# Performance work log

Measured on AMD Instinct MI355X. Metric: run time of the kernel, lower is better.

## Reference

```python
import jax, jax.numpy as jnp
import numpy as np

ROPE_THETA = 10000.0

def _rope(x, offset=0):
    # x: [B, H, T, d]; lucidrains rotary_embedding_torch interleaved-pair convention
    d = x.shape[-1]
    T = x.shape[-2]
    inv_freq = 1.0 / (ROPE_THETA ** (jnp.arange(0, d, 2, dtype=jnp.float32) / d))  # [d/2]
    t = jnp.arange(offset, offset + T, dtype=jnp.float32)
    freqs = t[:, None] * inv_freq[None, :]                 # [T, d/2]
    freqs = jnp.repeat(freqs, 2, axis=-1)                  # [T, d] (each freq duplicated for its pair)
    cos = jnp.cos(freqs).astype(x.dtype)
    sin = jnp.sin(freqs).astype(x.dtype)
    xr = x.reshape(*x.shape[:-1], d // 2, 2)
    x1, x2 = xr[..., 0], xr[..., 1]
    rot = jnp.stack([-x2, x1], axis=-1).reshape(x.shape)   # rotate_half, interleaved
    return x * cos + rot * sin


def setup_inputs() -> dict:
    key = jax.random.key(0)
    ks = jax.random.split(key, 5)
    B, T, C = 8, 1024, 1024
    s = 0.02
    x = jax.random.normal(ks[0], (B, T, C), dtype=jnp.float32)
    ipw = jax.random.normal(ks[1], (3 * C, C), dtype=jnp.float32) * s
    ipb = jax.random.normal(ks[2], (3 * C,), dtype=jnp.float32) * s
    opw = jax.random.normal(ks[3], (C, C), dtype=jnp.float32) * s
    opb = jax.random.normal(ks[4], (C,), dtype=jnp.float32) * s
    # bool mask, True = blocked (original code inverts before SDPA) -> causal
    causal_block = ~jnp.tril(jnp.ones((T, T), dtype=bool))
    attn_mask = causal_block[None, None, :, :]             # [1,1,T,T]
    return {"x": x, "ipw": ipw, "ipb": ipb, "opw": opw, "opb": opb,
            "attn_mask": attn_mask}


def reference(x, ipw, ipb, opw, opb, attn_mask):
    B, T, C = x.shape
    n_head = 16
    hd = C // n_head
    qkv = x @ ipw.T + ipb                                  # [B,T,3C]
    q, k, v = jnp.split(qkv, 3, axis=-1)
    def heads(z):
        return z.reshape(B, T, n_head, hd).transpose(0, 2, 1, 3)  # [B,H,T,hd]
    q, k, v = heads(q), heads(k), heads(v)
    q = _rope(q)
    k = _rope(k)
    scores = jnp.einsum('bhqd,bhkd->bhqk', q, k) / jnp.sqrt(jnp.asarray(hd, x.dtype))
    # attn_mask True = blocked; mask slice [FULL_T-T:FULL_T, :FULL_T] is the full mask here
    scores = jnp.where(attn_mask, jnp.asarray(-1e9, x.dtype), scores)
    attn = jax.nn.softmax(scores, axis=-1)
    y = jnp.einsum('bhqk,bhkd->bhqd', attn, v)             # [B,H,T,hd]
    y = y.transpose(0, 2, 1, 3).reshape(B, T, C)
    return y @ opw.T + opb
```

## Files before the change

kernel.cpp:

```cpp
#include <hip/hip_runtime.h>
#include <stdint.h>


typedef __bf16 bf16x8 __attribute__((ext_vector_type(8)));
typedef float f32x4 __attribute__((ext_vector_type(4)));
typedef __attribute__((address_space(1))) unsigned int as1_u32;
typedef __attribute__((address_space(3))) unsigned int as3_u32;

#define MFMA16(a, b, c) __builtin_amdgcn_mfma_f32_16x16x32_bf16((a), (b), (c), 0, 0, 0)

static __device__ __forceinline__ unsigned short f2bf(float f) {
    union { float f; unsigned u; } x; x.f = f;
    return (unsigned short)((x.u + 0x7fffu + ((x.u >> 16) & 1u)) >> 16);
}
static __device__ __forceinline__ float bf2f(unsigned short u) {
    union { unsigned u; float f; } x; x.u = ((unsigned)u) << 16;
    return x.f;
}
static __device__ __forceinline__ bf16x8 ld_bf16x8(const void* p) {
    return *(const bf16x8*)p;
}
static __device__ __forceinline__ unsigned cvtpk(float lo, float hi) {
    unsigned r;
    asm("v_cvt_pk_bf16_f32 %0, %1, %2" : "=v"(r) : "v"(lo), "v"(hi));
    return r;
}

__global__ void cast_f32_bf16(const float* __restrict__ in,
                              unsigned short* __restrict__ out, int n8) {
    int i = blockIdx.x * blockDim.x + threadIdx.x;
    if (i >= n8) return;
    float4 a = ((const float4*)in)[2 * i];
    float4 b = ((const float4*)in)[2 * i + 1];
    union { unsigned short us[8]; uint4 v; } o;
    o.us[0] = f2bf(a.x); o.us[1] = f2bf(a.y); o.us[2] = f2bf(a.z); o.us[3] = f2bf(a.w);
    o.us[4] = f2bf(b.x); o.us[5] = f2bf(b.y); o.us[6] = f2bf(b.z); o.us[7] = f2bf(b.w);
    ((uint4*)out)[i] = o.v;
}

__global__ void rope_table(float* __restrict__ ct, float* __restrict__ st) {
    int idx = blockIdx.x * blockDim.x + threadIdx.x;
    if (idx >= 1024 * 32) return;
    int t = idx >> 5, i = idx & 31;
    float inv = powf(10000.0f, -(float)(2 * i) * (1.0f / 64.0f));
    float f = (float)t * inv;
    ct[idx] = cosf(f);
    st[idx] = sinf(f);
}

__global__ __launch_bounds__(512, 2) void gemm1_8ph(const unsigned short* __restrict__ A,
                                                    const unsigned short* __restrict__ W,
                                                    const float* __restrict__ bias,
                                                    unsigned short* __restrict__ Cout) {
    __shared__ __attribute__((aligned(16))) char lds[131072];
    constexpr int NH = 32;
    constexpr int NTN = 12;

    int nwg = gridDim.x;
    int bid = blockIdx.x;
    int lg = (bid & 7) * (nwg >> 3) + (bid >> 3);
    int tm = lg / NTN, tn = lg % NTN;
    int m0 = tm * 256, n0 = tn * 256;

    int tid = threadIdx.x;
    int w = tid >> 6, l = tid & 63;
    int lr = l & 15, g = l >> 4;
    int wm = w >> 2, wn = w & 3;
    int ldsb = __builtin_amdgcn_readfirstlane(w * 1024);

    auto srcoff = [](int c) {
        int row = c >> 3;
        int sl = (c & 7) ^ (row & 7);
        int rg = (row << 1) | (sl >> 2);
        int cg = (sl & 3) * 8;
        return rg * 1024 + cg;
    };
    int c0 = tid, c1 = tid + 512;
    const unsigned short* pA0 = A + (size_t)m0 * 1024 + srcoff(c0);
    const unsigned short* pA1 = A + (size_t)m0 * 1024 + srcoff(c1);
    const unsigned short* pB0 = W + (size_t)n0 * 1024 + srcoff(c0);
    const unsigned short* pB1 = W + (size_t)n0 * 1024 + srcoff(c1);

    int lr2 = lr >> 1;
    int sst16 = ((((lr & 1) << 2) + g) ^ lr2) << 4;
    int aBase = (wm * 64 + lr2) * 128 + sst16;
    int bBase = (wn * 32 + lr2) * 128 + sst16;

    f32x4 acc[8][4] = {};

    for (int js = 0; js < 3; ++js) {
        char* Ad = lds + js * 16384;
        char* Bd = lds + 65536 + js * 16384;
        __builtin_amdgcn_global_load_lds((const as1_u32*)(pA0 + js * 32), (as3_u32*)(Ad + ldsb), 16, 0, 0);
        __builtin_amdgcn_global_load_lds((const as1_u32*)(pA1 + js * 32), (as3_u32*)(Ad + 8192 + ldsb), 16, 0, 0);
        __builtin_amdgcn_global_load_lds((const as1_u32*)(pB0 + js * 32), (as3_u32*)(Bd + ldsb), 16, 0, 0);
        __builtin_amdgcn_global_load_lds((const as1_u32*)(pB1 + js * 32), (as3_u32*)(Bd + 8192 + ldsb), 16, 0, 0);
    }
    asm volatile("s_waitcnt vmcnt(8)" ::: "memory");
    __builtin_amdgcn_s_barrier();

#pragma unroll 4
    for (int j = 0; j < NH; ++j) {
        const char* Asl = lds + (j & 3) * 16384;
        const char* Bsl = lds + 65536 + (j & 3) * 16384;
        int js = j + 3;
        char* Ad = lds + (js & 3) * 16384;
        char* Bd = lds + 65536 + (js & 3) * 16384;
        bf16x8 aa[4], bb[4];

#pragma unroll
        for (int fn = 0; fn < 4; ++fn) bb[fn] = ld_bf16x8(Bsl + bBase + fn * 1024);
#pragma unroll
        for (int fm = 0; fm < 4; ++fm) aa[fm] = ld_bf16x8(Asl + aBase + fm * 1024);
        if (js < NH) {
            __builtin_amdgcn_global_load_lds((const as1_u32*)(pA0 + js * 32), (as3_u32*)(Ad + ldsb), 16, 0, 0);
            __builtin_amdgcn_global_load_lds((const as1_u32*)(pA1 + js * 32), (as3_u32*)(Ad + 8192 + ldsb), 16, 0, 0);
        }
        __builtin_amdgcn_s_barrier();
        __builtin_amdgcn_s_setprio(1);
#pragma unroll
        for (int fm = 0; fm < 4; ++fm)
#pragma unroll
            for (int fn = 0; fn < 4; ++fn) acc[fm][fn] = MFMA16(aa[fm], bb[fn], acc[fm][fn]);
        __builtin_amdgcn_s_setprio(0);
        __builtin_amdgcn_s_barrier();

#pragma unroll
        for (int fm = 0; fm < 4; ++fm) aa[fm] = ld_bf16x8(Asl + aBase + (fm + 4) * 1024);
        if (js < NH) {
            __builtin_amdgcn_global_load_lds((const as1_u32*)(pB0 + js * 32), (as3_u32*)(Bd + ldsb), 16, 0, 0);
            __builtin_amdgcn_global_load_lds((const as1_u32*)(pB1 + js * 32), (as3_u32*)(Bd + 8192 + ldsb), 16, 0, 0);
        }
        __builtin_amdgcn_s_barrier();
        __builtin_amdgcn_s_setprio(1);
#pragma unroll
        for (int fm = 0; fm < 4; ++fm)
#pragma unroll
            for (int fn = 0; fn < 4; ++fn) acc[fm + 4][fn] = MFMA16(aa[fm], bb[fn], acc[fm + 4][fn]);
        __builtin_amdgcn_s_setprio(0);
        if (j + 3 < NH)      asm volatile("s_waitcnt vmcnt(8)" ::: "memory");
        else if (j + 2 < NH) asm volatile("s_waitcnt vmcnt(4)" ::: "memory");
        else if (j + 1 < NH) asm volatile("s_waitcnt vmcnt(0)" ::: "memory");
        __builtin_amdgcn_s_barrier();
    }

#pragma unroll
    for (int fn = 0; fn < 4; ++fn) {
        int col = n0 + wn * 64 + fn * 16 + lr;
        float bv = bias[col];
#pragma unroll
        for (int fm = 0; fm < 8; ++fm) {
            int row = m0 + wm * 128 + fm * 16 + g * 4;
#pragma unroll
            for (int r = 0; r < 4; ++r)
                Cout[(size_t)(row + r) * 3072 + col] = f2bf(acc[fm][fn][r] + bv);
        }
    }
}

template <int NC, bool OUT_BF16>
__global__ __launch_bounds__(256) void gemm_bt(const unsigned short* __restrict__ A,
                                               const unsigned short* __restrict__ W,
                                               const float* __restrict__ bias,
                                               void* __restrict__ Cout, int K) {
    __shared__ __attribute__((aligned(16))) unsigned short As[128 * 32];
    __shared__ __attribute__((aligned(16))) unsigned short Bs[128 * 32];

    constexpr int NT = NC / 128;
    int nwg = gridDim.x;
    int bid = blockIdx.x;
    int lg = (bid & 7) * (nwg >> 3) + (bid >> 3);
    int tm = lg / NT, tn = lg % NT;
    int m0 = tm * 128, n0 = tn * 128;

    int tid = threadIdx.x;
    int w = tid >> 6, l = tid & 63;
    int lr = l & 15, g = l >> 4;
    int ldsb = __builtin_amdgcn_readfirstlane(w * 512);

    int c0 = tid, c1 = tid + 256;
    const unsigned short* A0 = A + (size_t)(m0 + (c0 >> 2)) * K + (c0 & 3) * 8;
    const unsigned short* A1 = A + (size_t)(m0 + (c1 >> 2)) * K + (c1 & 3) * 8;
    const unsigned short* W0 = W + (size_t)(n0 + (c0 >> 2)) * K + (c0 & 3) * 8;
    const unsigned short* W1 = W + (size_t)(n0 + (c1 >> 2)) * K + (c1 & 3) * 8;

    f32x4 acc[4][4] = {};
    int wr = (w >> 1) * 64, wc = (w & 1) * 64;

    for (int k0 = 0; k0 < K; k0 += 32) {
        __syncthreads();
        __builtin_amdgcn_global_load_lds((const as1_u32*)(A0 + k0), (as3_u32*)(As + ldsb), 16, 0, 0);
        __builtin_amdgcn_global_load_lds((const as1_u32*)(A1 + k0), (as3_u32*)(As + 2048 + ldsb), 16, 0, 0);
        __builtin_amdgcn_global_load_lds((const as1_u32*)(W0 + k0), (as3_u32*)(Bs + ldsb), 16, 0, 0);
        __builtin_amdgcn_global_load_lds((const as1_u32*)(W1 + k0), (as3_u32*)(Bs + 2048 + ldsb), 16, 0, 0);
        __syncthreads();

        bf16x8 a[4], b[4];
#pragma unroll
        for (int i = 0; i < 4; ++i) a[i] = ld_bf16x8(As + (wr + i * 16 + lr) * 32 + g * 8);
#pragma unroll
        for (int j = 0; j < 4; ++j) b[j] = ld_bf16x8(Bs + (wc + j * 16 + lr) * 32 + g * 8);
#pragma unroll
        for (int i = 0; i < 4; ++i)
#pragma unroll
            for (int j = 0; j < 4; ++j) acc[i][j] = MFMA16(a[i], b[j], acc[i][j]);
    }

    int g4 = g * 4;
#pragma unroll
    for (int j = 0; j < 4; ++j) {
        int col = n0 + wc + j * 16 + lr;
        float bv = bias[col];
#pragma unroll
        for (int i = 0; i < 4; ++i) {
#pragma unroll
            for (int r = 0; r < 4; ++r) {
                int row = m0 + wr + i * 16 + g4 + r;
                float v = acc[i][j][r] + bv;
                if (OUT_BF16)
                    ((unsigned short*)Cout)[(size_t)row * NC + col] = f2bf(v);
                else
                    ((float*)Cout)[(size_t)row * NC + col] = v;
            }
        }
    }
}

__global__ void rope_reshape(const unsigned short* __restrict__ qkv,
                             const float* __restrict__ ct, const float* __restrict__ st,
                             unsigned short* __restrict__ Qh,
                             unsigned short* __restrict__ Kh) {
    int idx = blockIdx.x * blockDim.x + threadIdx.x;
    if (idx >= 8192 * 256) return;
    int row = idx >> 8;
    int col = (idx & 255) * 8;
    int sec = col >> 10;
    int wi = col & 1023;
    int h = wi >> 6, d = wi & 63;
    int t = row & 1023;

    uint4 raw = *(const uint4*)(qkv + (size_t)row * 3072 + col);
    size_t obase = ((size_t)((row >> 10) * 16 + h) * 1024 + t) * 64 + d;

    union { uint4 v; unsigned short us[8]; } u; u.v = raw;
    float x[8];
#pragma unroll
    for (int i = 0; i < 8; ++i) x[i] = bf2f(u.us[i]);
    float scale = (sec == 0) ? 0.125f : 1.0f;
    union { uint4 v; unsigned short us[8]; } o;
#pragma unroll
    for (int p = 0; p < 4; ++p) {
        int fi = t * 32 + (d >> 1) + p;
        float c = ct[fi], s = st[fi];
        float e0 = (x[2 * p] * c - x[2 * p + 1] * s) * scale;
        float e1 = (x[2 * p + 1] * c + x[2 * p] * s) * scale;
        o.us[2 * p] = f2bf(e0);
        o.us[2 * p + 1] = f2bf(e1);
    }
    unsigned short* dst = (sec == 0) ? Qh : Kh;
    *(uint4*)(dst + obase) = o.v;
}

__global__ __launch_bounds__(256) void transpose_v(const unsigned short* __restrict__ qkv,
                                                   unsigned short* __restrict__ Vt) {
    __shared__ unsigned short Ts[64 * 67];
    int bid = blockIdx.x;
    int bh = bid >> 4, tt = bid & 15;
    int b = bh >> 4, h = bh & 15;
    int t0 = tt * 64;
    int tid = threadIdx.x;
#pragma unroll
    for (int cc = 0; cc < 2; ++cc) {
        int c = tid + cc * 256;
        int trow = c >> 3, d8 = (c & 7) * 8;
        uint4 v = *(const uint4*)(qkv + (size_t)(b * 1024 + t0 + trow) * 3072 + 2048 + h * 64 + d8);
        union { uint4 v; unsigned short us[8]; } u; u.v = v;
#pragma unroll
        for (int i = 0; i < 8; ++i) Ts[trow * 67 + d8 + i] = u.us[i];
    }
    __syncthreads();
#pragma unroll
    for (int cc = 0; cc < 2; ++cc) {
        int c = tid + cc * 256;
        int drow = c >> 3, t8 = (c & 7) * 8;
        union { uint4 v; unsigned short us[8]; } u;
#pragma unroll
        for (int i = 0; i < 8; ++i) u.us[i] = Ts[(t8 + i) * 67 + drow];
        *(uint4*)(Vt + (size_t)bh * 65536 + (size_t)drow * 1024 + t0 + t8) = u.v;
    }
}

__device__ __forceinline__ void attn_tile(const unsigned short* Ks, const unsigned short* Vs,
                                          bf16x8 q0f, bf16x8 q1f, f32x4 (&y)[4],
                                          float& rm, float& rl,
                                          int lr, int g, bool diag, int wq) {
    const char* kc = (const char*)Ks;
    const char* vc = (const char*)Vs;
    int l7 = lr & 7;
    int kof0 = lr * 128 + ((g ^ l7) << 4);
    int kof1 = lr * 128 + (((g + 4) ^ l7) << 4);
    f32x4 s[4];
#pragma unroll
    for (int nt = 0; nt < 4; ++nt) {
        bf16x8 kf0 = ld_bf16x8(kc + nt * 2048 + kof0);
        bf16x8 kf1 = ld_bf16x8(kc + nt * 2048 + kof1);
        f32x4 z = {};
        z = MFMA16(kf0, q0f, z);
        z = MFMA16(kf1, q1f, z);
        s[nt] = z;
    }
    if (diag) {
#pragma unroll
        for (int nt = 0; nt < 4; ++nt)
#pragma unroll
            for (int r = 0; r < 4; ++r)
                if (nt * 16 + g * 4 + r > wq + lr) s[nt][r] = -3e38f;
    }
    float tm;
    {
        f32x4 m4;
#pragma unroll
        for (int r = 0; r < 4; ++r) m4[r] = fmaxf(fmaxf(s[0][r], s[1][r]), fmaxf(s[2][r], s[3][r]));
        tm = fmaxf(fmaxf(m4[0], m4[1]), fmaxf(m4[2], m4[3]));
    }
    tm = fmaxf(tm, __shfl_xor(tm, 16));
    tm = fmaxf(tm, __shfl_xor(tm, 32));
    float nm = fmaxf(rm, tm);
    float alpha = __expf(rm - nm);
    rm = nm;
    float ts = 0.f;
#pragma unroll
    for (int nt = 0; nt < 4; ++nt)
#pragma unroll
        for (int r = 0; r < 4; ++r) { float pv = __expf(s[nt][r] - nm); s[nt][r] = pv; ts += pv; }
    ts += __shfl_xor(ts, 16);
    ts += __shfl_xor(ts, 32);
    rl = rl * alpha + ts;
#pragma unroll
    for (int nt = 0; nt < 4; ++nt) y[nt] *= alpha;
    union { unsigned u[4]; bf16x8 v; } pf0, pf1;
    pf0.u[0] = cvtpk(s[0][0], s[0][1]); pf0.u[1] = cvtpk(s[0][2], s[0][3]);
    pf0.u[2] = cvtpk(s[1][0], s[1][1]); pf0.u[3] = cvtpk(s[1][2], s[1][3]);
    pf1.u[0] = cvtpk(s[2][0], s[2][1]); pf1.u[1] = cvtpk(s[2][2], s[2][3]);
    pf1.u[2] = cvtpk(s[3][0], s[3][1]); pf1.u[3] = cvtpk(s[3][2], s[3][3]);
    int s0 = g >> 1, h8 = (g & 1) * 8;
    int vo0 = lr * 128 + h8 + (((s0 + 0) ^ l7) << 4);
    int vo1 = lr * 128 + h8 + (((s0 + 2) ^ l7) << 4);
    int vo2 = lr * 128 + h8 + (((s0 + 4) ^ l7) << 4);
    int vo3 = lr * 128 + h8 + (((s0 + 6) ^ l7) << 4);
#pragma unroll
    for (int nt = 0; nt < 4; ++nt) {
        union { uint2 u2[2]; bf16x8 v; } vf;
        vf.u2[0] = *(const uint2*)(vc + nt * 2048 + vo0);
        vf.u2[1] = *(const uint2*)(vc + nt * 2048 + vo1);
        y[nt] = MFMA16(vf.v, pf0.v, y[nt]);
        union { uint2 u2[2]; bf16x8 v; } vg;
        vg.u2[0] = *(const uint2*)(vc + nt * 2048 + vo2);
        vg.u2[1] = *(const uint2*)(vc + nt * 2048 + vo3);
        y[nt] = MFMA16(vg.v, pf1.v, y[nt]);
    }
}

__device__ __forceinline__ void attn_epilogue(unsigned short* smem, unsigned short* __restrict__ Yb,
                                              f32x4 (&y)[4], float rl, int qtile,
                                              int b, int hh, int w, int lr, int g, int tid) {
    __syncthreads();
    float inv = 1.0f / rl;
    char* ep = (char*)smem;
#pragma unroll
    for (int nt = 0; nt < 4; ++nt) {
        uint2 pr;
        pr.x = cvtpk(y[nt][0] * inv, y[nt][1] * inv);
        pr.y = cvtpk(y[nt][2] * inv, y[nt][3] * inv);
        *(uint2*)(ep + (w * 16 + lr) * 144 + (nt * 16 + g * 4) * 2) = pr;
    }
    __syncthreads();
    int q = tid >> 2, dc = (tid & 3) * 16;
    uint4 u0 = *(const uint4*)(ep + q * 144 + dc * 2);
    uint4 u1 = *(const uint4*)(ep + q * 144 + dc * 2 + 16);
    size_t orow = ((size_t)(b * 1024 + qtile * 64 + q)) * 1024 + hh * 64 + dc;
    *(uint4*)(Yb + orow) = u0;
    *(uint4*)(Yb + orow + 8) = u1;
}

__global__ __launch_bounds__(256) void attn_fwd(const unsigned short* __restrict__ Qh,
                                                const unsigned short* __restrict__ Kh,
                                                const unsigned short* __restrict__ Vt,
                                                unsigned short* __restrict__ Yb) {
    __shared__ __attribute__((aligned(16))) unsigned short smem[8192];
    unsigned short* Ks = smem;
    unsigned short* Vs = smem + 4096;

    int bid = blockIdx.x;
    int lg = (bid & 7) * 128 + (bid >> 3);
    int bh = lg >> 3, p = lg & 7;
    int qa = p, qb = 15 - p;

    int tid = threadIdx.x, w = tid >> 6, l = tid & 63;
    int lr = l & 15, g = l >> 4;
    int ldsb = __builtin_amdgcn_readfirstlane(w * 512);

    size_t bh64 = (size_t)bh * 65536;
    const unsigned short* qbase = Qh + bh64 + (size_t)(w * 16 + lr) * 64 + g * 8;
    bf16x8 qA0 = ld_bf16x8(qbase + qa * 4096);
    bf16x8 qA1 = ld_bf16x8(qbase + qa * 4096 + 32);
    bf16x8 qB0 = ld_bf16x8(qbase + qb * 4096);
    bf16x8 qB1 = ld_bf16x8(qbase + qb * 4096 + 32);

    f32x4 yA[4] = {}, yB[4] = {};
    float mA = -3e38f, lA = 0.f, mB = -3e38f, lB = 0.f;

    int c0 = tid, c1 = tid + 256;
    const unsigned short* K0 = Kh + bh64 + (c0 >> 3) * 64 + ((c0 ^ (c0 >> 3)) & 7) * 8;
    const unsigned short* K1 = Kh + bh64 + (c1 >> 3) * 64 + ((c1 ^ (c1 >> 3)) & 7) * 8;
    const unsigned short* V0 = Vt + bh64 + (c0 >> 3) * 1024 + ((c0 ^ (c0 >> 3)) & 7) * 8;
    const unsigned short* V1 = Vt + bh64 + (c1 >> 3) * 1024 + ((c1 ^ (c1 >> 3)) & 7) * 8;

    for (int t = 0; t <= qb; ++t) {
        __syncthreads();
        __builtin_amdgcn_global_load_lds((const as1_u32*)(K0 + t * 4096), (as3_u32*)(Ks + ldsb), 16, 0, 0);
        __builtin_amdgcn_global_load_lds((const as1_u32*)(K1 + t * 4096), (as3_u32*)(Ks + 2048 + ldsb), 16, 0, 0);
        __builtin_amdgcn_global_load_lds((const as1_u32*)(V0 + t * 64), (as3_u32*)(Vs + ldsb), 16, 0, 0);
        __builtin_amdgcn_global_load_lds((const as1_u32*)(V1 + t * 64), (as3_u32*)(Vs + 2048 + ldsb), 16, 0, 0);
        __syncthreads();

        if (t <= qa)
            attn_tile(Ks, Vs, qA0, qA1, yA, mA, lA, lr, g, t == qa, w * 16);
        attn_tile(Ks, Vs, qB0, qB1, yB, mB, lB, lr, g, t == qb, w * 16);
    }

    int b = bh >> 4, hh = bh & 15;
    attn_epilogue(smem, Yb, yA, lA, qa, b, hh, w, lr, g, tid);
    attn_epilogue(smem, Yb, yB, lB, qb, b, hh, w, lr, g, tid);
}

extern "C" void kernel_launch(void* const* d_in, const int* in_sizes, int n_in,
                              void* d_out, int out_size, void* d_ws, size_t ws_size,
                              hipStream_t stream) {
    const float* x = (const float*)d_in[0];
    const float* ipw = (const float*)d_in[1];
    const float* ipb = (const float*)d_in[2];
    const float* opw = (const float*)d_in[3];
    const float* opb = (const float*)d_in[4];

    char* ws = (char*)d_ws;
    unsigned short* xb   = (unsigned short*)(ws);
    unsigned short* wqkv = (unsigned short*)(ws + 16777216);
    unsigned short* wo   = (unsigned short*)(ws + 23068672);
    float* ct            = (float*)(ws + 25165824);
    float* st            = (float*)(ws + 25296896);
    unsigned short* qkvb = (unsigned short*)(ws + 25427968);
    unsigned short* Qh   = (unsigned short*)(ws + 75759616);
    unsigned short* Kh   = (unsigned short*)(ws + 92536832);
    unsigned short* Vt   = (unsigned short*)(ws + 109314048);
    unsigned short* yb   = (unsigned short*)(ws + 126091264);

    cast_f32_bf16<<<4096, 256, 0, stream>>>(x, xb, 1048576);
    cast_f32_bf16<<<1536, 256, 0, stream>>>(ipw, wqkv, 393216);
    cast_f32_bf16<<<512, 256, 0, stream>>>(opw, wo, 131072);
    rope_table<<<128, 256, 0, stream>>>(ct, st);

    gemm1_8ph<<<384, 512, 0, stream>>>(xb, wqkv, ipb, qkvb);
    rope_reshape<<<8192, 256, 0, stream>>>(qkvb, ct, st, Qh, Kh);
    transpose_v<<<2048, 256, 0, stream>>>(qkvb, Vt);
    attn_fwd<<<1024, 256, 0, stream>>>(Qh, Kh, Vt, yb);
    gemm_bt<1024, false><<<512, 256, 0, stream>>>(yb, wo, opb, d_out, 1024);
}
```

Before: 277.3 us.

## Widen QKV GEMM tile to 256x384 with triple-buffered LDS and staged epilogue

The QKV projection GEMM tile grows from 256x256 to 256x384, cutting the grid from 384 to 256 workgroups, which matches the 256 CUs, and raising MFMA work per A-fragment load. LDS buffering changes from a 4-slot ring to 3 rotating buffers to fit the larger B tile. The epilogue now stages bf16 results through swizzled LDS so it can issue 16-byte coalesced global stores instead of scattered 2-byte stores. The cost is more accumulator registers (48 f32x4 per thread), which adds register pressure and can hurt occupancy, plus only two k-steps of prefetch in flight.

```diff
diff --git a/kernel.cpp b/kernel.cpp
--- a/kernel.cpp
+++ b/kernel.cpp
@@ -52,15 +52,14 @@
                                                     const unsigned short* __restrict__ W,
                                                     const float* __restrict__ bias,
                                                     unsigned short* __restrict__ Cout) {
-    __shared__ __attribute__((aligned(16))) char lds[131072];
+    __shared__ __attribute__((aligned(16))) char lds[122880];
     constexpr int NH = 32;
-    constexpr int NTN = 12;
 
     int nwg = gridDim.x;
     int bid = blockIdx.x;
     int lg = (bid & 7) * (nwg >> 3) + (bid >> 3);
-    int tm = lg / NTN, tn = lg % NTN;
-    int m0 = tm * 256, n0 = tn * 256;
+    int tm = lg >> 3, tn = lg & 7;
+    int m0 = tm * 256, n0 = tn * 384;
 
     int tid = threadIdx.x;
     int w = tid >> 6, l = tid & 63;
@@ -75,85 +74,104 @@
         int cg = (sl & 3) * 8;
         return rg * 1024 + cg;
     };
-    int c0 = tid, c1 = tid + 512;
-    const unsigned short* pA0 = A + (size_t)m0 * 1024 + srcoff(c0);
-    const unsigned short* pA1 = A + (size_t)m0 * 1024 + srcoff(c1);
-    const unsigned short* pB0 = W + (size_t)n0 * 1024 + srcoff(c0);
-    const unsigned short* pB1 = W + (size_t)n0 * 1024 + srcoff(c1);
+    const unsigned short* pA0 = A + (size_t)m0 * 1024 + srcoff(tid);
+    const unsigned short* pA1 = A + (size_t)m0 * 1024 + srcoff(tid + 512);
+    const unsigned short* pB0 = W + (size_t)n0 * 1024 + srcoff(tid);
+    const unsigned short* pB1 = W + (size_t)n0 * 1024 + srcoff(tid + 512);
+    const unsigned short* pB2 = W + (size_t)n0 * 1024 + srcoff(tid + 1024);
 
     int lr2 = lr >> 1;
     int sst16 = ((((lr & 1) << 2) + g) ^ lr2) << 4;
     int aBase = (wm * 64 + lr2) * 128 + sst16;
-    int bBase = (wn * 32 + lr2) * 128 + sst16;
-
-    f32x4 acc[8][4] = {};
-
-    for (int js = 0; js < 3; ++js) {
-        char* Ad = lds + js * 16384;
-        char* Bd = lds + 65536 + js * 16384;
-        __builtin_amdgcn_global_load_lds((const as1_u32*)(pA0 + js * 32), (as3_u32*)(Ad + ldsb), 16, 0, 0);
-        __builtin_amdgcn_global_load_lds((const as1_u32*)(pA1 + js * 32), (as3_u32*)(Ad + 8192 + ldsb), 16, 0, 0);
-        __builtin_amdgcn_global_load_lds((const as1_u32*)(pB0 + js * 32), (as3_u32*)(Bd + ldsb), 16, 0, 0);
-        __builtin_amdgcn_global_load_lds((const as1_u32*)(pB1 + js * 32), (as3_u32*)(Bd + 8192 + ldsb), 16, 0, 0);
-    }
-    asm volatile("s_waitcnt vmcnt(8)" ::: "memory");
+    int bBase = (wn * 48 + lr2) * 128 + sst16;
+
+    f32x4 acc[8][6] = {};
+
+    int aC = 0, aN = 16384, aP = 32768;
+    int bC = 49152, bN = 73728, bP = 98304;
+
+    __builtin_amdgcn_global_load_lds((const as1_u32*)(pA0), (as3_u32*)(lds + aC + ldsb), 16, 0, 0);
+    __builtin_amdgcn_global_load_lds((const as1_u32*)(pA1), (as3_u32*)(lds + aC + 8192 + ldsb), 16, 0, 0);
+    __builtin_amdgcn_global_load_lds((const as1_u32*)(pB0), (as3_u32*)(lds + bC + ldsb), 16, 0, 0);
+    __builtin_amdgcn_global_load_lds((const as1_u32*)(pB1), (as3_u32*)(lds + bC + 8192 + ldsb), 16, 0, 0);
+    __builtin_amdgcn_global_load_lds((const as1_u32*)(pB2), (as3_u32*)(lds + bC + 16384 + ldsb), 16, 0, 0);
+    __builtin_amdgcn_global_load_lds((const as1_u32*)(pA0 + 32), (as3_u32*)(lds + aN + ldsb), 16, 0, 0);
+    __builtin_amdgcn_global_load_lds((const as1_u32*)(pA1 + 32), (as3_u32*)(lds + aN + 8192 + ldsb), 16, 0, 0);
+    __builtin_amdgcn_global_load_lds((const as1_u32*)(pB0 + 32), (as3_u32*)(lds + bN + ldsb), 16, 0, 0);
+    __builtin_amdgcn_global_load_lds((const as1_u32*)(pB1 + 32), (as3_u32*)(lds + bN + 8192 + ldsb), 16, 0, 0);
+    __builtin_amdgcn_global_load_lds((const as1_u32*)(pB2 + 32), (as3_u32*)(lds + bN + 16384 + ldsb), 16, 0, 0);
+    asm volatile("s_waitcnt vmcnt(5)" ::: "memory");
     __builtin_amdgcn_s_barrier();
 
-#pragma unroll 4
+#pragma unroll
     for (int j = 0; j < NH; ++j) {
-        const char* Asl = lds + (j & 3) * 16384;
-        const char* Bsl = lds + 65536 + (j & 3) * 16384;
-        int js = j + 3;
-        char* Ad = lds + (js & 3) * 16384;
-        char* Bd = lds + 65536 + (js & 3) * 16384;
-        bf16x8 aa[4], bb[4];
-
-#pragma unroll
-        for (int fn = 0; fn < 4; ++fn) bb[fn] = ld_bf16x8(Bsl + bBase + fn * 1024);
+        const char* Asl = lds + aC;
+        const char* Bsl = lds + bC;
+        int ko = (j + 2) * 32;
+        bool st = (j + 2) < NH;
+        bf16x8 aa[4], bb[6];
+
+#pragma unroll
+        for (int fn = 0; fn < 6; ++fn) bb[fn] = ld_bf16x8(Bsl + bBase + fn * 1024);
 #pragma unroll
         for (int fm = 0; fm < 4; ++fm) aa[fm] = ld_bf16x8(Asl + aBase + fm * 1024);
-        if (js < NH) {
-            __builtin_amdgcn_global_load_lds((const as1_u32*)(pA0 + js * 32), (as3_u32*)(Ad + ldsb), 16, 0, 0);
-            __builtin_amdgcn_global_load_lds((const as1_u32*)(pA1 + js * 32), (as3_u32*)(Ad + 8192 + ldsb), 16, 0, 0);
+        if (st) {
+            __builtin_amdgcn_global_load_lds((const as1_u32*)(pA0 + ko), (as3_u32*)(lds + aP + ldsb), 16, 0, 0);
+            __builtin_amdgcn_global_load_lds((const as1_u32*)(pA1 + ko), (as3_u32*)(lds + aP + 8192 + ldsb), 16, 0, 0);
         }
         __builtin_amdgcn_s_barrier();
         __builtin_amdgcn_s_setprio(1);
 #pragma unroll
         for (int fm = 0; fm < 4; ++fm)
 #pragma unroll
-            for (int fn = 0; fn < 4; ++fn) acc[fm][fn] = MFMA16(aa[fm], bb[fn], acc[fm][fn]);
+            for (int fn = 0; fn < 6; ++fn) acc[fm][fn] = MFMA16(aa[fm], bb[fn], acc[fm][fn]);
         __builtin_amdgcn_s_setprio(0);
         __builtin_amdgcn_s_barrier();
 
 #pragma unroll
         for (int fm = 0; fm < 4; ++fm) aa[fm] = ld_bf16x8(Asl + aBase + (fm + 4) * 1024);
-        if (js < NH) {
-            __builtin_amdgcn_global_load_lds((const as1_u32*)(pB0 + js * 32), (as3_u32*)(Bd + ldsb), 16, 0, 0);
-            __builtin_amdgcn_global_load_lds((const as1_u32*)(pB1 + js * 32), (as3_u32*)(Bd + 8192 + ldsb), 16, 0, 0);
+        if (st) {
+            __builtin_amdgcn_global_load_lds((const as1_u32*)(pB0 + ko), (as3_u32*)(lds + bP + ldsb), 16, 0, 0);
+            __builtin_amdgcn_global_load_lds((const as1_u32*)(pB1 + ko), (as3_u32*)(lds + bP + 8192 + ldsb), 16, 0, 0);
+            __builtin_amdgcn_global_load_lds((const as1_u32*)(pB2 + ko), (as3_u32*)(lds + bP + 16384 + ldsb), 16, 0, 0);
         }
         __builtin_amdgcn_s_barrier();
         __builtin_amdgcn_s_setprio(1);
 #pragma unroll
         for (int fm = 0; fm < 4; ++fm)
 #pragma unroll
-            for (int fn = 0; fn < 4; ++fn) acc[fm + 4][fn] = MFMA16(aa[fm], bb[fn], acc[fm + 4][fn]);
+            for (int fn = 0; fn < 6; ++fn) acc[fm + 4][fn] = MFMA16(aa[fm], bb[fn], acc[fm + 4][fn]);
         __builtin_amdgcn_s_setprio(0);
-        if (j + 3 < NH)      asm volatile("s_waitcnt vmcnt(8)" ::: "memory");
-        else if (j + 2 < NH) asm volatile("s_waitcnt vmcnt(4)" ::: "memory");
-        else if (j + 1 < NH) asm volatile("s_waitcnt vmcnt(0)" ::: "memory");
+        if (st)                 asm volatile("s_waitcnt vmcnt(5)" ::: "memory");
+        else if (j + 2 == NH)   asm volatile("s_waitcnt vmcnt(0)" ::: "memory");
         __builtin_amdgcn_s_barrier();
-    }
-
-#pragma unroll
-    for (int fn = 0; fn < 4; ++fn) {
-        int col = n0 + wn * 64 + fn * 16 + lr;
-        float bv = bias[col];
-#pragma unroll
-        for (int fm = 0; fm < 8; ++fm) {
-            int row = m0 + wm * 128 + fm * 16 + g * 4;
+
+        int t = aC; aC = aN; aN = aP; aP = t;
+        t = bC; bC = bN; bN = bP; bP = t;
+    }
+
+    __syncthreads();
+    char* ep = lds + w * 3072;
+    float bv[6];
+#pragma unroll
+    for (int fn = 0; fn < 6; ++fn) bv[fn] = bias[n0 + wn * 96 + fn * 16 + lr];
+#pragma unroll
+    for (int fm = 0; fm < 8; ++fm) {
+#pragma unroll
+        for (int fn = 0; fn < 6; ++fn)
 #pragma unroll
             for (int r = 0; r < 4; ++r)
-                Cout[(size_t)(row + r) * 3072 + col] = f2bf(acc[fm][fn][r] + bv);
+                *(unsigned short*)(ep + (g * 4 + r) * 192 + (((fn * 16 + lr) * 2) ^ (g << 4))) =
+                    f2bf(acc[fm][fn][r] + bv[fn]);
+        asm volatile("s_waitcnt lgkmcnt(0)" ::: "memory");
+        __builtin_amdgcn_sched_barrier(0);
+#pragma unroll
+        for (int i = 0; i < 3; ++i) {
+            int c = l + 64 * i;
+            int row = c / 12, ch = c - row * 12;
+            int swz = (row & 12) << 2;
+            uint4 v = *(const uint4*)(ep + row * 192 + ((ch * 16) ^ swz));
+            *(uint4*)(Cout + (size_t)(m0 + wm * 128 + fm * 16 + row) * 3072 + (n0 + wn * 96 + ch * 8)) = v;
         }
     }
 }
@@ -460,7 +478,7 @@
     cast_f32_bf16<<<512, 256, 0, stream>>>(opw, wo, 131072);
     rope_table<<<128, 256, 0, stream>>>(ct, st);
 
-    gemm1_8ph<<<384, 512, 0, stream>>>(xb, wqkv, ipb, qkvb);
+    gemm1_8ph<<<256, 512, 0, stream>>>(xb, wqkv, ipb, qkvb);
     rope_reshape<<<8192, 256, 0, stream>>>(qkvb, ct, st, Qh, Kh);
     transpose_v<<<2048, 256, 0, stream>>>(qkvb, Vt);
     attn_fwd<<<1024, 256, 0, stream>>>(Qh, Kh, Vt, yb);
```

New measurement: 265.5 us. -4.2%, faster.
